# Kernel tuning notes

Hardware: AMD Instinct MI355X
Metric: run time of the kernel (lower is better)

Reference implementation:

```python
import jax, jax.numpy as jnp
import numpy as np

T_SIG = 400        # current-waveform ticks per (track, pixel)
T_TOTAL = 10000    # total time ticks in the accumulated pixel signal
ADC_SAMPLE = 50    # ticks integrated per ADC sample (the `* 50` in the source)
GAIN = 0.25        # affine digitization gain (stand-in for mV/e conversion)
PEDESTAL = 74.0    # ADC pedestal
ADC_MAX = 255.0    # 8-bit ADC saturation
GRID = 128         # pixel plane is GRID x GRID


def setup_inputs() -> dict:
    rng = np.random.default_rng(0)
    N, M, U = 3000, 16, 8192
    # U distinct pixel coordinates on a GRID x GRID plane (the `unique_pix` list)
    flat = rng.permutation(GRID * GRID)[:U]
    pool = np.stack([flat // GRID, flat % GRID], axis=1).astype(np.int32)  # [U, 2]
    # each track touches M neighboring pixels drawn from the plane
    idx = rng.integers(0, U, size=(N, M))
    neigh = pool[idx].copy()  # [N, M, 2]
    dead = rng.random((N, M)) < 0.05
    neigh[dead] = -1
    signals = rng.standard_normal((N, M, T_SIG)).astype(np.float32)
    track_starts = rng.integers(0, T_TOTAL - T_SIG, size=N).astype(np.int32)
    return {
        "neighboring_pixels": jnp.asarray(neigh),
        "unique_pix": jnp.asarray(pool),
        "signals": jnp.asarray(signals),
        "track_starts": jnp.asarray(track_starts),
    }


def reference(neighboring_pixels, unique_pix, signals, track_starts):
    N, M, T = signals.shape
    U = unique_pix.shape[0]
    # --- pixel index map via full broadcast compare, as in the source ---
    # eq: [N, M, U] boolean, matching coords on both axes
    eq = (neighboring_pixels[:, :, None, 0] == unique_pix[None, None, :, 0]) & \
         (neighboring_pixels[:, :, None, 1] == unique_pix[None, None, :, 1])
    any_match = eq.any(axis=-1)
    # unmatched / (-1,-1) entries routed to dummy row U (dropped after scatter)
    pixel_index_map = jnp.where(any_match, jnp.argmax(eq, axis=-1), U)  # [N, M]
    # --- sum_pixel_signals: scatter-accumulate waveforms at track start offsets ---
    pixels_signals = jnp.zeros((U + 1, T_TOTAL), dtype=signals.dtype)
    cols = track_starts[:, None] + jnp.arange(T, dtype=track_starts.dtype)  # [N, T]
    pixels_signals = pixels_signals.at[
        pixel_index_map[:, :, None],  # [N, M, 1]
        cols[:, None, :],             # [N, 1, T]
    ].add(signals)
    pixels_signals = pixels_signals[:U]  # drop dummy row
    # --- get_adc_values + digitize (integrate, sample every ADC_SAMPLE ticks, affine+clip) ---
    csum = jnp.cumsum(pixels_signals, axis=1)                 # [U, T_TOTAL]
    integrals = csum[:, ADC_SAMPLE - 1::ADC_SAMPLE]           # [U, T_TOTAL // ADC_SAMPLE]
    adc = jnp.clip(integrals * GAIN + PEDESTAL, 0.0, ADC_MAX)
    return adc
```

## Files before the change

kernel.cpp:

```cpp
#include <hip/hip_runtime.h>

#define GRID_DIM  128
#define T_SIG     400
#define NSAMP     200
#define WIN       50
#define GAIN      0.25f
#define PEDESTAL  74.0f
#define ADC_MAX   255.0f


__global__ __launch_bounds__(256)
void scatter_windows(const int* __restrict__ neigh,
                     const float* __restrict__ signals,
                     const int* __restrict__ track_starts,
                     float* __restrict__ Wg,
                     int n_tasks, int M) {
    int wave = blockIdx.x * (blockDim.x >> 6) + (threadIdx.x >> 6);
    int lane = threadIdx.x & 63;
    if (wave >= n_tasks) return;

    int px = neigh[2 * wave];
    int py = neigh[2 * wave + 1];
    if (px < 0) return;
    int row = px * GRID_DIM + py;

    int s  = track_starts[wave / M];
    int k0 = s / WIN;
    int nw = (s + T_SIG - 1) / WIN - k0 + 1;

    float chunk = 0.f;
    float bsum  = 0.f;
    if (lane < T_SIG / 8) {
        const float4* sig4 = (const float4*)signals;
        int b = wave * (T_SIG / 4) + 2 * lane;
        float4 a = sig4[b];
        float4 c = sig4[b + 1];
        float e[8] = {a.x, a.y, a.z, a.w, c.x, c.y, c.z, c.w};
        int g = s + 8 * lane;
        int r = g % WIN;
        int t = (WIN - r) % WIN;
        #pragma unroll
        for (int j = 0; j < 8; ++j) {
            chunk += e[j];
            if (j < t) bsum += e[j];
        }
    }

    float cs = chunk;
    #pragma unroll
    for (int off = 1; off < 64; off <<= 1) {
        float v = __shfl_up(cs, off, 64);
        if (lane >= off) cs += v;
    }
    float bval  = (cs - chunk) + bsum;
    float total = __shfl(cs, T_SIG / 8 - 1, 64);

    int o_lo = (k0 + lane) * WIN - s;
    int o_hi = o_lo + WIN;
    int src_lo = (o_lo > 0 && o_lo < T_SIG) ? (o_lo >> 3) : 0;
    int src_hi = (o_hi > 0 && o_hi < T_SIG) ? (o_hi >> 3) : 0;
    float p_lo = __shfl(bval, src_lo, 64);
    float p_hi = __shfl(bval, src_hi, 64);
    if (o_lo <= 0)        p_lo = 0.f;
    if (o_hi >= T_SIG)    p_hi = total;

    if (lane < nw)
        atomicAdd(&Wg[(size_t)row * NSAMP + k0 + lane], p_hi - p_lo);
}

__global__ __launch_bounds__(256)
void scan_adc(const float* __restrict__ Wg,
              const int* __restrict__ unique_pix,
              float* __restrict__ out, int U) {
    int u    = blockIdx.x * (blockDim.x >> 6) + (threadIdx.x >> 6);
    int lane = threadIdx.x & 63;
    if (u >= U) return;

    int x = unique_pix[2 * u];
    int y = unique_pix[2 * u + 1];
    const float* rowp = Wg + (size_t)(x * GRID_DIM + y) * NSAMP;

    float4 v = make_float4(0.f, 0.f, 0.f, 0.f);
    if (lane < NSAMP / 4)
        v = ((const float4*)rowp)[lane];

    float s0 = v.x;
    float s1 = s0 + v.y;
    float s2 = s1 + v.z;
    float s3 = s2 + v.w;

    float cs = s3;
    #pragma unroll
    for (int off = 1; off < 64; off <<= 1) {
        float t = __shfl_up(cs, off, 64);
        if (lane >= off) cs += t;
    }
    float base = cs - s3;

    if (lane < NSAMP / 4) {
        float4 o;
        o.x = fminf(fmaxf((base + s0) * GAIN + PEDESTAL, 0.f), ADC_MAX);
        o.y = fminf(fmaxf((base + s1) * GAIN + PEDESTAL, 0.f), ADC_MAX);
        o.z = fminf(fmaxf((base + s2) * GAIN + PEDESTAL, 0.f), ADC_MAX);
        o.w = fminf(fmaxf((base + s3) * GAIN + PEDESTAL, 0.f), ADC_MAX);
        ((float4*)(out + (size_t)u * NSAMP))[lane] = o;
    }
}

extern "C" void kernel_launch(void* const* d_in, const int* in_sizes, int n_in,
                              void* d_out, int out_size, void* d_ws, size_t ws_size,
                              hipStream_t stream) {
    const int*   neigh        = (const int*)d_in[0];
    const int*   unique_pix   = (const int*)d_in[1];
    const float* signals      = (const float*)d_in[2];
    const int*   track_starts = (const int*)d_in[3];
    float*       out          = (float*)d_out;

    int N = in_sizes[3];
    int M = in_sizes[0] / (2 * N);
    int U = in_sizes[1] / 2;

    float* Wg = (float*)d_ws;

    int n_tasks = N * M;
    scatter_windows<<<(n_tasks + 3) / 4, 256, 0, stream>>>(neigh, signals,
                                                           track_starts, Wg,
                                                           n_tasks, M);

    scan_adc<<<(U + 3) / 4, 256, 0, stream>>>(Wg, unique_pix, out, U);
}
```

Before: 122.0 us.

## Accumulate into compact per-unique-pixel buffer and use DPP wave scans

A small kernel now builds an inverse map from grid coordinate to unique-pixel index. The scatter kernel atomically accumulates ADC windows into a compact U-row buffer instead of a full GRID*GRID buffer, so the scan kernel reads rows contiguously without the coordinate indirection. The shuffle-based prefix scans are replaced with DPP row-shift and broadcast adds plus a readlane, and the track index uses a shift when M is a power of two. In exchange it adds a kernel launch and an inverse-map lookup per task, and it assumes every valid neighbor coordinate appears in unique_pix.

New measurement: 121.9 us. Within noise of the previous version (-0.1%).

```diff
diff --git a/kernel.cpp b/kernel.cpp
--- a/kernel.cpp
+++ b/kernel.cpp
@@ -9,22 +9,50 @@
 #define ADC_MAX   255.0f
 
 
+template<int CTRL, int RMASK>
+__device__ __forceinline__ float dpp_add(float x) {
+    int xi = __builtin_bit_cast(int, x);
+    int sh = __builtin_amdgcn_update_dpp(0, xi, CTRL, RMASK, 0xF, true);
+    return x + __builtin_bit_cast(float, sh);
+}
+
+__device__ __forceinline__ float wave_incl_scan(float x) {
+    x = dpp_add<0x111, 0xF>(x);
+    x = dpp_add<0x112, 0xF>(x);
+    x = dpp_add<0x114, 0xF>(x);
+    x = dpp_add<0x118, 0xF>(x);
+    x = dpp_add<0x142, 0xA>(x);
+    x = dpp_add<0x143, 0xC>(x);
+    return x;
+}
+
+__global__ __launch_bounds__(256)
+void build_inv(const int* __restrict__ up, int* __restrict__ inv, int U) {
+    int u = blockIdx.x * 256 + threadIdx.x;
+    if (u < U) {
+        int x = up[2 * u];
+        int y = up[2 * u + 1];
+        inv[x * GRID_DIM + y] = u;
+    }
+}
+
 __global__ __launch_bounds__(256)
 void scatter_windows(const int* __restrict__ neigh,
                      const float* __restrict__ signals,
                      const int* __restrict__ track_starts,
-                     float* __restrict__ Wg,
-                     int n_tasks, int M) {
-    int wave = blockIdx.x * (blockDim.x >> 6) + (threadIdx.x >> 6);
+                     const int* __restrict__ inv,
+                     float* __restrict__ Wc,
+                     int n_tasks, int M, int mshift) {
+    int wave = blockIdx.x * (256 >> 6) + (threadIdx.x >> 6);
     int lane = threadIdx.x & 63;
     if (wave >= n_tasks) return;
 
-    int px = neigh[2 * wave];
-    int py = neigh[2 * wave + 1];
-    if (px < 0) return;
-    int row = px * GRID_DIM + py;
+    int2 pp = ((const int2*)neigh)[wave];
+    if (pp.x < 0) return;
+    int u = inv[pp.x * GRID_DIM + pp.y];
 
-    int s  = track_starts[wave / M];
+    int tr = (mshift >= 0) ? (wave >> mshift) : (wave / M);
+    int s  = track_starts[tr];
     int k0 = s / WIN;
     int nw = (s + T_SIG - 1) / WIN - k0 + 1;
 
@@ -46,14 +74,10 @@
         }
     }
 
-    float cs = chunk;
-    #pragma unroll
-    for (int off = 1; off < 64; off <<= 1) {
-        float v = __shfl_up(cs, off, 64);
-        if (lane >= off) cs += v;
-    }
-    float bval  = (cs - chunk) + bsum;
-    float total = __shfl(cs, T_SIG / 8 - 1, 64);
+    float cs   = wave_incl_scan(chunk);
+    float bval = (cs - chunk) + bsum;
+    float total = __builtin_bit_cast(float,
+        __builtin_amdgcn_readlane(__builtin_bit_cast(int, cs), T_SIG / 8 - 1));
 
     int o_lo = (k0 + lane) * WIN - s;
     int o_hi = o_lo + WIN;
@@ -65,36 +89,26 @@
     if (o_hi >= T_SIG)    p_hi = total;
 
     if (lane < nw)
-        atomicAdd(&Wg[(size_t)row * NSAMP + k0 + lane], p_hi - p_lo);
+        atomicAdd(&Wc[(size_t)u * NSAMP + k0 + lane], p_hi - p_lo);
 }
 
 __global__ __launch_bounds__(256)
-void scan_adc(const float* __restrict__ Wg,
-              const int* __restrict__ unique_pix,
+void scan_adc(const float* __restrict__ Wc,
               float* __restrict__ out, int U) {
-    int u    = blockIdx.x * (blockDim.x >> 6) + (threadIdx.x >> 6);
+    int u    = blockIdx.x * (256 >> 6) + (threadIdx.x >> 6);
     int lane = threadIdx.x & 63;
     if (u >= U) return;
 
-    int x = unique_pix[2 * u];
-    int y = unique_pix[2 * u + 1];
-    const float* rowp = Wg + (size_t)(x * GRID_DIM + y) * NSAMP;
-
     float4 v = make_float4(0.f, 0.f, 0.f, 0.f);
     if (lane < NSAMP / 4)
-        v = ((const float4*)rowp)[lane];
+        v = ((const float4*)(Wc + (size_t)u * NSAMP))[lane];
 
     float s0 = v.x;
     float s1 = s0 + v.y;
     float s2 = s1 + v.z;
     float s3 = s2 + v.w;
 
-    float cs = s3;
-    #pragma unroll
-    for (int off = 1; off < 64; off <<= 1) {
-        float t = __shfl_up(cs, off, 64);
-        if (lane >= off) cs += t;
-    }
+    float cs   = wave_incl_scan(s3);
     float base = cs - s3;
 
     if (lane < NSAMP / 4) {
@@ -120,12 +134,18 @@
     int M = in_sizes[0] / (2 * N);
     int U = in_sizes[1] / 2;
 
-    float* Wg = (float*)d_ws;
+    float* Wc  = (float*)d_ws;
+    int*   inv = (int*)((char*)d_ws + (size_t)U * NSAMP * sizeof(float));
+
+    int mshift = ((M & (M - 1)) == 0) ? __builtin_ctz(M) : -1;
+
+    build_inv<<<(U + 255) / 256, 256, 0, stream>>>(unique_pix, inv, U);
 
     int n_tasks = N * M;
     scatter_windows<<<(n_tasks + 3) / 4, 256, 0, stream>>>(neigh, signals,
-                                                           track_starts, Wg,
-                                                           n_tasks, M);
+                                                           track_starts, inv,
+                                                           Wc, n_tasks, M,
+                                                           mshift);
 
-    scan_adc<<<(U + 3) / 4, 256, 0, stream>>>(Wg, unique_pix, out, U);
+    scan_adc<<<(U + 3) / 4, 256, 0, stream>>>(Wc, out, U);
 }
```
